# Performance work log

Hardware: AMD Instinct MI355X
Metric: run time of the kernel (lower is better)

## Reference

```python
import jax, jax.numpy as jnp
import numpy as np

B, N, C, NSAMPLE = 4, 1024, 512, 32
RADIUS, HMIN, HMAX = 0.05, -0.02, 0.04
EPS = 1e-5


def setup_inputs() -> dict:
    key = jax.random.key(0)
    ks = jax.random.split(key, 6)
    # points in a ~20cm cube so the 5cm cylinder actually captures neighbors
    seed_xyz_graspable = jax.random.uniform(ks[0], (B, N, 3), jnp.float32) * 0.2
    seed_features_graspable = jax.random.normal(ks[1], (B, C, N), jnp.float32)
    rot_raw = jax.random.normal(ks[2], (B, N, 3, 3), jnp.float32)
    vp_rot, _ = jnp.linalg.qr(rot_raw)  # proper-ish per-seed view rotations
    W1 = jax.random.normal(ks[3], (512, 3 + C), jnp.float32) / np.float32(np.sqrt(3 + C))
    g1 = jnp.ones((512,), jnp.float32)
    b1 = jnp.zeros((512,), jnp.float32)
    W2 = jax.random.normal(ks[4], (512, 512), jnp.float32) / np.float32(np.sqrt(512))
    g2 = jnp.ones((512,), jnp.float32)
    b2 = jnp.zeros((512,), jnp.float32)
    return dict(seed_xyz_graspable=seed_xyz_graspable,
                seed_features_graspable=seed_features_graspable,
                vp_rot=vp_rot, W1=W1, g1=g1, b1=b1, W2=W2, g2=g2, b2=b2)


def _cylinder_query(xyz, rot):
    # offsets d[b,m,n] = xyz[b,n] - query[b,m], rotated into the cylinder frame (d @ R)
    d = xyz[:, None, :, :] - xyz[:, :, None, :]                 # (B,M,N,3)
    r = jnp.einsum('bmnd,bmde->bmne', d, rot)                   # (B,M,N,3)
    mask = (r[..., 1] ** 2 + r[..., 2] ** 2 < RADIUS ** 2) \
         & (r[..., 0] > HMIN) & (r[..., 0] < HMAX)              # (B,M,N)
    # first NSAMPLE valid indices; pad with the first valid index (CUDA kernel semantics)
    cand = jnp.where(mask, jnp.arange(N, dtype=jnp.int32)[None, None, :], N)
    idx = jnp.sort(cand, axis=-1)[..., :NSAMPLE]                # (B,M,S)
    idx = jnp.where(idx == N, idx[..., :1], idx)
    return idx


def _bn_relu(x, g, b):
    # training-mode BatchNorm2d over (B, M, S) per output channel; x: (B,O,M,S)
    mean = jnp.mean(x, axis=(0, 2, 3), keepdims=True)
    var = jnp.var(x, axis=(0, 2, 3), keepdims=True)
    xn = (x - mean) * jax.lax.rsqrt(var + EPS)
    return jax.nn.relu(xn * g[None, :, None, None] + b[None, :, None, None])


def reference(seed_xyz_graspable, seed_features_graspable, vp_rot, W1, g1, b1, W2, g2, b2):
    xyz = seed_xyz_graspable                                    # (B,N,3)
    idx = _cylinder_query(xyz, vp_rot)                          # (B,M,S) int32
    # gather neighbor coordinates and center/rotate/normalize
    grouped_xyz = jnp.take_along_axis(xyz[:, None], idx[..., None], axis=2)   # (B,M,S,3)
    local = grouped_xyz - xyz[:, :, None, :]
    local = jnp.einsum('bmsd,bmde->bmse', local, vp_rot) / RADIUS             # normalize_xyz
    # gather neighbor features
    feats = jnp.swapaxes(seed_features_graspable, 1, 2)                       # (B,N,C)
    gfeat = jnp.take_along_axis(feats[:, None], idx[..., None], axis=2)       # (B,M,S,C)
    x = jnp.concatenate([local, gfeat], axis=-1)                              # (B,M,S,3+C)
    # SharedMLP: 1x1 conv (no bias) + BN + ReLU, twice; channels-first layout (B,O,M,S)
    h = _bn_relu(jnp.einsum('bmsc,oc->boms', x, W1), g1, b1)
    h = _bn_relu(jnp.einsum('boms,po->bpms', h, W2), g2, b2)
    # max-pool over the nsample axis -> (B,512,M)
    return jnp.max(h, axis=-1)
```

## Files before the change

kernel.cpp:

```cpp
#include <hip/hip_runtime.h>
#include <hip/hip_bf16.h>
#include <stdint.h>

#define BATCH 4
#define NPTS  1024
#define CIN   512
#define NS    32
#define P_TOT (BATCH*NPTS*NS)
#define CO    512
#define RADIUS_F 0.05f
#define HMIN_F  (-0.02f)
#define HMAX_F  (0.04f)

typedef __attribute__((ext_vector_type(8))) short short8;
typedef __attribute__((ext_vector_type(4))) float f32x4;

__device__ __forceinline__ unsigned short f2bf(float f) {
  unsigned int x = __float_as_uint(f);
  x = x + 0x7fffu + ((x >> 16) & 1u);
  return (unsigned short)(x >> 16);
}
__device__ __forceinline__ float bf2f(unsigned short u) {
  return __uint_as_float(((unsigned int)u) << 16);
}
__device__ __forceinline__ unsigned int cvtpk(float lo, float hi) {
  unsigned int r;
  asm("v_cvt_pk_bf16_f32 %0, %1, %2" : "=v"(r) : "v"(lo), "v"(hi));
  return r;
}
__device__ __forceinline__ void load_lds16(const void* g, void* l) {
  __builtin_amdgcn_global_load_lds((const __attribute__((address_space(1))) void*)g,
                                   (__attribute__((address_space(3))) void*)l, 16, 0, 0);
}

__global__ __launch_bounds__(256) void pre_kernel(
    const float* __restrict__ feats, const float* __restrict__ W1,
    const float* __restrict__ W2, const float* __restrict__ xyz,
    const float* __restrict__ rot,
    unsigned short* __restrict__ featsT, unsigned short* __restrict__ w1f,
    float* __restrict__ w1l, unsigned short* __restrict__ w2b,
    int* __restrict__ idxout, float* __restrict__ lxyz,
    float* __restrict__ L4, float* __restrict__ GMP) {
  __shared__ float tile[64][65];
  __shared__ int sidx[4][32];
  int bx = blockIdx.x;
  int t = threadIdx.x;
  if (bx < 512) {
    int nb = bx & 15, cb = (bx >> 4) & 7, b = bx >> 7;
    int tr = t >> 6, tc = t & 63;
    #pragma unroll
    for (int j = 0; j < 16; ++j) {
      int c = cb*64 + j*4 + tr;
      tile[j*4+tr][tc] = feats[((size_t)b*CIN + c)*NPTS + nb*64 + tc];
    }
    __syncthreads();
    #pragma unroll
    for (int j = 0; j < 16; ++j) {
      int n = nb*64 + j*4 + tr;
      featsT[((size_t)b*NPTS + n)*CIN + cb*64 + tc] = f2bf(tile[tc][j*4+tr]);
    }
  } else if (bx < 1536) {
    int i = (bx - 512)*256 + t;
    int o = i >> 9, k = i & 511;
    w1f[i] = f2bf(W1[o*515 + 3 + k]);
    w2b[i] = f2bf(W2[i]);
    if (i < 1536) w1l[i] = W1[(i/3)*515 + (i%3)];
  } else {
    int w = t >> 6, lane = t & 63;
    int bm = (bx - 1536)*4 + w;
    int b = bm >> 10;
    const float* ctr = xyz + (size_t)bm * 3;
    float cx = ctr[0], cy = ctr[1], cz = ctr[2];
    const float* R = rot + (size_t)bm * 9;
    float r00=R[0],r01=R[1],r02=R[2],r10=R[3],r11=R[4],r12=R[5],r20=R[6],r21=R[7],r22=R[8];
    int taken = 0;
    for (int base = 0; base < NPTS && taken < NS; base += 64) {
      int n = base + lane;
      const float* p = xyz + ((size_t)b * NPTS + n) * 3;
      float dx = p[0]-cx, dy = p[1]-cy, dz = p[2]-cz;
      float rx = dx*r00 + dy*r10 + dz*r20;
      float ry = dx*r01 + dy*r11 + dz*r21;
      float rz = dx*r02 + dy*r12 + dz*r22;
      bool ok = (ry*ry + rz*rz < RADIUS_F*RADIUS_F) && (rx > HMIN_F) && (rx < HMAX_F);
      unsigned long long bal = __ballot(ok);
      if (ok) {
        int slot = taken + __popcll(bal & ((1ull << lane) - 1ull));
        if (slot < NS) sidx[w][slot] = n;
      }
      taken += __popcll(bal);
    }
    __syncthreads();
    int filled = taken < NS ? taken : NS;
    float m[9] = {0.f,0.f,0.f,0.f,0.f,0.f,0.f,0.f,0.f};
    if (lane < NS) {
      int nsel = (lane < filled) ? sidx[w][lane] : sidx[w][0];
      size_t pp = (size_t)bm * NS + lane;
      idxout[pp] = nsel;
      const float* pn = xyz + ((size_t)b * NPTS + nsel) * 3;
      float dx = pn[0]-cx, dy = pn[1]-cy, dz = pn[2]-cz;
      const float inv = 1.0f / RADIUS_F;
      float rx = (dx*r00 + dy*r10 + dz*r20) * inv;
      float ry = (dx*r01 + dy*r11 + dz*r21) * inv;
      float rz = (dx*r02 + dy*r12 + dz*r22) * inv;
      float* lw = lxyz + pp * 3;
      lw[0] = rx; lw[1] = ry; lw[2] = rz;
      float* dst = L4 + (((size_t)b << 10) + nsel)*4;
      atomicAdd(dst+0, rx); atomicAdd(dst+1, ry);
      atomicAdd(dst+2, rz); atomicAdd(dst+3, 1.0f);
      m[0]=rx; m[1]=ry; m[2]=rz;
      m[3]=rx*rx; m[4]=rx*ry; m[5]=rx*rz; m[6]=ry*ry; m[7]=ry*rz; m[8]=rz*rz;
    }
    #pragma unroll
    for (int d = 1; d < 64; d <<= 1)
      #pragma unroll
      for (int e = 0; e < 9; ++e) m[e] += __shfl_xor(m[e], d);
    if (lane < 9) atomicAdd(&GMP[(bm & 31)*12 + lane], m[lane]);
  }
}

__global__ __launch_bounds__(256) void gemm1u_kernel(
    const unsigned short* __restrict__ A,
    const unsigned short* __restrict__ Bw,
    float* __restrict__ C,
    const float* __restrict__ L4,
    const float* __restrict__ w1l,
    float* __restrict__ sums)
{
  __shared__ unsigned short As[64*32];
  __shared__ unsigned short Bs[64*32];
  int bx = blockIdx.x;
  int ob = bx & 7;
  size_t p0 = (size_t)(bx >> 3) * 64;
  int o0 = ob * 64;
  int t = threadIdx.x;
  int w = t >> 6, lane = t & 63;
  int wr = w >> 1, wc = w & 1;
  int l15 = lane & 15, l4 = lane >> 4;
  f32x4 acc[2][2];
  f32x4 zf = {0.f, 0.f, 0.f, 0.f};
  #pragma unroll
  for (int mi = 0; mi < 2; ++mi)
    #pragma unroll
    for (int ni = 0; ni < 2; ++ni) acc[mi][ni] = zf;

  int srow = t >> 2;
  int scol = (t & 3) * 8;
  const unsigned short* abase = A + (p0 + srow)*(size_t)512 + scol;
  const unsigned short* bbase = Bw + (size_t)(o0 + srow)*512 + scol;

  for (int k0 = 0; k0 < 512; k0 += 32) {
    load_lds16(abase + k0, (char*)As + w*1024);
    load_lds16(bbase + k0, (char*)Bs + w*1024);
    __syncthreads();
    short8 af[2], bfr[2];
    #pragma unroll
    for (int mi = 0; mi < 2; ++mi)
      af[mi] = *(const short8*)(As + (wr*32 + mi*16 + l15)*32 + l4*8);
    #pragma unroll
    for (int ni = 0; ni < 2; ++ni)
      bfr[ni] = *(const short8*)(Bs + (wc*32 + ni*16 + l15)*32 + l4*8);
    #pragma unroll
    for (int mi = 0; mi < 2; ++mi)
      #pragma unroll
      for (int ni = 0; ni < 2; ++ni)
        acc[mi][ni] = __builtin_amdgcn_mfma_f32_16x16x32_bf16(af[mi], bfr[ni], acc[mi][ni], 0, 0, 0);
    __syncthreads();
  }
  #pragma unroll
  for (int mi = 0; mi < 2; ++mi)
    #pragma unroll
    for (int ni = 0; ni < 2; ++ni)
      #pragma unroll
      for (int j = 0; j < 4; ++j) {
        size_t p = p0 + wr*32 + mi*16 + l4*4 + j;
        int o = o0 + wc*32 + ni*16 + l15;
        C[p*512 + o] = acc[mi][ni][j];
      }
  #pragma unroll
  for (int ni = 0; ni < 2; ++ni) {
    int c = o0 + wc*32 + ni*16 + l15;
    float wa = w1l[c*3], wb = w1l[c*3+1], wcc = w1l[c*3+2];
    float s = 0.f, q = 0.f;
    #pragma unroll
    for (int mi = 0; mi < 2; ++mi)
      #pragma unroll
      for (int j = 0; j < 4; ++j) {
        size_t p = p0 + wr*32 + mi*16 + l4*4 + j;
        float4 L = *(const float4*)(L4 + p*4);
        float h = acc[mi][ni][j];
        float lw = L.x*wa + L.y*wb + L.z*wcc;
        s += L.w*h;
        q += L.w*h*h + 2.f*h*lw;
      }
    s += __shfl_xor(s, 16); q += __shfl_xor(q, 16);
    s += __shfl_xor(s, 32); q += __shfl_xor(q, 32);
    if (l4 == 0) {
      atomicAdd(&sums[c], s);
      atomicAdd(&sums[512 + c], q);
    }
  }
}

__global__ __launch_bounds__(256) void fold_fin_kernel(
    float* __restrict__ h1u,
    const float* __restrict__ sums,
    const float* __restrict__ GMP,
    const float* __restrict__ w1l,
    const float* __restrict__ g,
    const float* __restrict__ bia,
    float* __restrict__ w1ls) {
  __shared__ float ssl[1024];
  __shared__ float gms[9];
  int t = threadIdx.x;
  if (t < 9) {
    float s = 0.f;
    #pragma unroll
    for (int k = 0; k < 32; ++k) s += GMP[k*12 + t];
    gms[t] = s;
  }
  __syncthreads();
  #pragma unroll
  for (int cc = t; cc < 512; cc += 256) {
    float w0 = w1l[cc*3], w1 = w1l[cc*3+1], w2 = w1l[cc*3+2];
    float S = sums[cc] + w0*gms[0] + w1*gms[1] + w2*gms[2];
    float Q = sums[512+cc] + w0*w0*gms[3] + 2.f*w0*w1*gms[4] + 2.f*w0*w2*gms[5]
                           + w1*w1*gms[6] + 2.f*w1*w2*gms[7] + w2*w2*gms[8];
    const float invN = 1.f / (float)P_TOT;
    float mean = S * invN;
    float var  = Q * invN - mean*mean;
    float sc = g[cc] * rsqrtf(var + 1e-5f);
    ssl[cc] = sc;
    ssl[512+cc] = bia[cc] - mean*sc;
    if (blockIdx.x == 0) {
      w1ls[cc]        = sc * w0;
      w1ls[512 + cc]  = sc * w1;
      w1ls[1024 + cc] = sc * w2;
    }
  }
  __syncthreads();
  size_t i = ((size_t)blockIdx.x*256 + t) * 4;
  int c = (int)(i & 511);
  float4 v = *(float4*)(h1u + i);
  v.x = fmaf(v.x, ssl[c],   ssl[512+c]);
  v.y = fmaf(v.y, ssl[c+1], ssl[512+c+1]);
  v.z = fmaf(v.z, ssl[c+2], ssl[512+c+2]);
  v.w = fmaf(v.w, ssl[c+3], ssl[512+c+3]);
  *(float4*)(h1u + i) = v;
}

__global__ __launch_bounds__(512) void gemm2_kernel(
    const float* __restrict__ h1u,
    const int* __restrict__ idx,
    const float* __restrict__ lxyz,
    const float* __restrict__ w1ls,
    const unsigned short* __restrict__ Bw,
    float* __restrict__ sums,
    float* __restrict__ pmax,
    float* __restrict__ pmin)
{
  __shared__ unsigned short As[128*32];
  __shared__ unsigned short Bs[256*32];
  __shared__ float wl[1536];
  int bx = blockIdx.x;
  int ob = bx & 1;
  size_t p0 = (size_t)(bx >> 1) * 128;
  int o0 = ob * 256;
  int t = threadIdx.x;
  int w = t >> 6, lane = t & 63;
  int wr = w >> 2;
  int wc = w & 3;
  int l15 = lane & 15, l4 = lane >> 4;
  f32x4 acc[4][4];
  f32x4 zf = {0.f, 0.f, 0.f, 0.f};
  #pragma unroll
  for (int mi = 0; mi < 4; ++mi)
    #pragma unroll
    for (int ni = 0; ni < 4; ++ni) acc[mi][ni] = zf;

  int sl = (lane & 3) ^ ((lane >> 3) & 3);
  int scole = (lane & 3) * 8;
  int cA = (l4 ^ ((l15 >> 1) & 3)) * 8;

  wl[t] = w1ls[t]; wl[512 + t] = w1ls[512 + t]; wl[1024 + t] = w1ls[1024 + t];

  int arow = 16*w + (lane >> 2);
  int awoff = arow*64 + sl*16;
  const float* hptr;
  float lxr, lyr, lzr;
  {
    size_t p = p0 + arow;
    int b = (int)(p >> 15);
    int n = idx[p];
    hptr = h1u + (((size_t)b << 10) + n)*512 + scole;
    const float* lwp = lxyz + p*3;
    lxr = lwp[0]; lyr = lwp[1]; lzr = lwp[2];
  }
  const unsigned short* bptr[2];
  #pragma unroll
  for (int cc = 0; cc < 2; ++cc) {
    int brow = 16*(2*w + cc) + (lane >> 2);
    bptr[cc] = Bw + (size_t)(o0 + brow)*CIN + sl*8;
  }

  float4 hv0 = *(const float4*)(hptr);
  float4 hv1 = *(const float4*)(hptr + 4);
  __syncthreads();

  for (int k0 = 0; k0 < CIN; k0 += 32) {
    #pragma unroll
    for (int cc = 0; cc < 2; ++cc)
      load_lds16(bptr[cc] + k0, (char*)Bs + (2*w + cc)*1024);
    int ch0 = k0 + scole;
    float4 xa = *(const float4*)(wl + ch0);
    float4 xb = *(const float4*)(wl + ch0 + 4);
    float4 ya = *(const float4*)(wl + 512 + ch0);
    float4 yb = *(const float4*)(wl + 512 + ch0 + 4);
    float4 za = *(const float4*)(wl + 1024 + ch0);
    float4 zb = *(const float4*)(wl + 1024 + ch0 + 4);
    float w0[8] = {xa.x,xa.y,xa.z,xa.w,xb.x,xb.y,xb.z,xb.w};
    float w1[8] = {ya.x,ya.y,ya.z,ya.w,yb.x,yb.y,yb.z,yb.w};
    float w2[8] = {za.x,za.y,za.z,za.w,zb.x,zb.y,zb.z,zb.w};
    {
      float fv[8] = {hv0.x, hv0.y, hv0.z, hv0.w, hv1.x, hv1.y, hv1.z, hv1.w};
      float gv[8];
      #pragma unroll
      for (int e = 0; e < 8; ++e)
        gv[e] = fmaxf(fv[e] + lxr*w0[e] + lyr*w1[e] + lzr*w2[e], 0.f);
      unsigned int rv[4];
      #pragma unroll
      for (int j = 0; j < 4; ++j) rv[j] = cvtpk(gv[2*j], gv[2*j+1]);
      *(uint4*)((char*)As + awoff) = make_uint4(rv[0], rv[1], rv[2], rv[3]);
    }
    if (k0 + 32 < CIN) {
      hv0 = *(const float4*)(hptr + k0 + 32);
      hv1 = *(const float4*)(hptr + k0 + 36);
    }
    __syncthreads();
    short8 af[4], bfr[4];
    #pragma unroll
    for (int mi = 0; mi < 4; ++mi)
      af[mi] = *(const short8*)(As + (wr*64 + mi*16 + l15)*32 + cA);
    #pragma unroll
    for (int ni = 0; ni < 4; ++ni)
      bfr[ni] = *(const short8*)(Bs + (wc*64 + ni*16 + l15)*32 + cA);
    #pragma unroll
    for (int mi = 0; mi < 4; ++mi)
      #pragma unroll
      for (int ni = 0; ni < 4; ++ni)
        acc[mi][ni] = __builtin_amdgcn_mfma_f32_16x16x32_bf16(af[mi], bfr[ni], acc[mi][ni], 0, 0, 0);
    __syncthreads();
  }

  #pragma unroll
  for (int ni = 0; ni < 4; ++ni) {
    float s = 0.f, q = 0.f;
    #pragma unroll
    for (int mi = 0; mi < 4; ++mi)
      #pragma unroll
      for (int j = 0; j < 4; ++j) { float v = acc[mi][ni][j]; s += v; q += v*v; }
    s += __shfl_xor(s, 16); q += __shfl_xor(q, 16);
    s += __shfl_xor(s, 32); q += __shfl_xor(q, 32);
    if (l4 == 0) {
      int c = o0 + wc*64 + ni*16 + l15;
      atomicAdd(&sums[c], s);
      atomicAdd(&sums[512 + c], q);
    }
  }
  #pragma unroll
  for (int ni = 0; ni < 4; ++ni) {
    #pragma unroll
    for (int h = 0; h < 2; ++h) {
      float mx = -3.4e38f, mn = 3.4e38f;
      #pragma unroll
      for (int mi = 2*h; mi < 2*h + 2; ++mi)
        #pragma unroll
        for (int j = 0; j < 4; ++j) {
          float v = acc[mi][ni][j];
          mx = fmaxf(mx, v); mn = fminf(mn, v);
        }
      mx = fmaxf(mx, __shfl_xor(mx, 16)); mn = fminf(mn, __shfl_xor(mn, 16));
      mx = fmaxf(mx, __shfl_xor(mx, 32)); mn = fminf(mn, __shfl_xor(mn, 32));
      if (l4 == 0) {
        size_t bm = (p0 >> 5) + 2*wr + h;
        int o = o0 + wc*64 + ni*16 + l15;
        pmax[bm*512 + o] = mx;
        pmin[bm*512 + o] = mn;
      }
    }
  }
}

__global__ void final_transpose(const float* __restrict__ pmax,
                                const float* __restrict__ pmin,
                                const float* __restrict__ sums,
                                const float* __restrict__ g,
                                const float* __restrict__ bia,
                                float* __restrict__ out) {
  __shared__ float tile[64][65];
  __shared__ float scl[64], shl[64];
  int b = blockIdx.z, ob = blockIdx.y, mb = blockIdx.x;
  int t = threadIdx.x, tr = t >> 6, tc = t & 63;
  if (t < 64) {
    int c = ob*64 + t;
    const float invN = 1.f / (float)P_TOT;
    float mean = sums[c] * invN;
    float var  = sums[512+c] * invN - mean*mean;
    float sc = g[c] * rsqrtf(var + 1e-5f);
    scl[t] = sc;
    shl[t] = bia[c] - mean*sc;
  }
  __syncthreads();
  #pragma unroll
  for (int j = 0; j < 16; ++j) {
    int m = mb*64 + j*4 + tr;
    float sc = scl[tc], sh = shl[tc];
    size_t pi = (((size_t)b << 10) + m)*512 + ob*64 + tc;
    float v = (sc >= 0.f) ? pmax[pi] : pmin[pi];
    tile[j*4+tr][tc] = fmaxf(fmaf(v, sc, sh), 0.f);
  }
  __syncthreads();
  #pragma unroll
  for (int j = 0; j < 16; ++j) {
    int o = ob*64 + j*4 + tr;
    out[((size_t)b*512 + o)*1024 + mb*64 + tc] = tile[tc][j*4+tr];
  }
}

extern "C" void kernel_launch(void* const* d_in, const int* in_sizes, int n_in,
                              void* d_out, int out_size, void* d_ws, size_t ws_size,
                              hipStream_t stream) {
  const float* xyz   = (const float*)d_in[0];
  const float* feats = (const float*)d_in[1];
  const float* rot   = (const float*)d_in[2];
  const float* W1    = (const float*)d_in[3];
  const float* g1    = (const float*)d_in[4];
  const float* b1    = (const float*)d_in[5];
  const float* W2    = (const float*)d_in[6];
  const float* g2    = (const float*)d_in[7];
  const float* b2    = (const float*)d_in[8];
  float* out = (float*)d_out;
  char* wsb = (char*)d_ws;

  const size_t OFF_IDX    = 0;
  const size_t OFF_LXYZ   = OFF_IDX    + (size_t)P_TOT*4;
  const size_t OFF_FEATST = OFF_LXYZ   + (size_t)P_TOT*3*4;
  const size_t OFF_W1F    = OFF_FEATST + (size_t)BATCH*NPTS*CIN*2;
  const size_t OFF_W1L    = OFF_W1F    + (size_t)CO*512*2;
  const size_t OFF_W1LS   = OFF_W1L    + 8192;
  const size_t OFF_W2B    = OFF_W1LS   + 8192;
  const size_t OFF_STATS  = OFF_W2B    + (size_t)CO*CIN*2;
  const size_t OFF_L4     = OFF_STATS  + 16384;
  const size_t OFF_GMP    = OFF_L4     + 65536;
  const size_t OFF_H1U    = OFF_GMP    + 4096;
  const size_t OFF_PMAX   = OFF_H1U    + (size_t)BATCH*NPTS*CO*4;
  const size_t OFF_PMIN   = OFF_PMAX   + (size_t)BATCH*NPTS*CO*4;
  const size_t WS_NEED    = OFF_PMIN   + (size_t)BATCH*NPTS*CO*4;

  if (ws_size < WS_NEED) return;

  int* idx             = (int*)(wsb + OFF_IDX);
  float* lxyz          = (float*)(wsb + OFF_LXYZ);
  unsigned short* fT   = (unsigned short*)(wsb + OFF_FEATST);
  unsigned short* w1f  = (unsigned short*)(wsb + OFF_W1F);
  float* w1l           = (float*)(wsb + OFF_W1L);
  float* w1ls          = (float*)(wsb + OFF_W1LS);
  unsigned short* w2b  = (unsigned short*)(wsb + OFF_W2B);
  float* stats         = (float*)(wsb + OFF_STATS);
  float* sums1 = stats;
  float* sums2 = stats + 2048;
  float* L4            = (float*)(wsb + OFF_L4);
  float* GMP           = (float*)(wsb + OFF_GMP);
  float* h1u           = (float*)(wsb + OFF_H1U);
  float* pmax          = (float*)(wsb + OFF_PMAX);
  float* pmin          = (float*)(wsb + OFF_PMIN);

  hipMemsetAsync(stats, 0, 16384 + 65536 + 4096, stream);

  pre_kernel<<<2560, 256, 0, stream>>>(feats, W1, W2, xyz, rot,
                                       fT, w1f, w1l, w2b, idx, lxyz, L4, GMP);

  gemm1u_kernel<<<512, 256, 0, stream>>>(fT, w1f, h1u, L4, w1l, sums1);

  fold_fin_kernel<<<(BATCH*NPTS*CO/4)/256, 256, 0, stream>>>(h1u, sums1, GMP,
                                                             w1l, g1, b1, w1ls);

  gemm2_kernel<<<(P_TOT/128)*2, 512, 0, stream>>>(h1u, idx, lxyz, w1ls, w2b,
                                                  sums2, pmax, pmin);

  final_transpose<<<dim3(NPTS/64, CO/64, BATCH), 256, 0, stream>>>(pmax, pmin,
                                                                   sums2, g2, b2, out);
}
```

Baseline: 194.1 us.

## Double-buffer B tile and prefetch A inputs two steps ahead in gemm2

Splits the LDS B tile into two buffers so the next K-slice's weights load asynchronously while MFMAs run on the current slice. The A-tile transform for the next slice is computed in registers during the current iteration, and the global h1 loads are issued two steps ahead. The goal is to hide global-to-LDS latency behind matrix math. In exchange the B tile uses twice the LDS, register pressure rises, and each iteration still has two barriers because As is single-buffered.

```diff
diff --git a/kernel.cpp b/kernel.cpp
--- a/kernel.cpp
+++ b/kernel.cpp
@@ -259,7 +259,7 @@
     float* __restrict__ pmin)
 {
   __shared__ unsigned short As[128*32];
-  __shared__ unsigned short Bs[256*32];
+  __shared__ unsigned short Bs[2][256*32];
   __shared__ float wl[1536];
   int bx = blockIdx.x;
   int ob = bx & 1;
@@ -302,15 +302,7 @@
     bptr[cc] = Bw + (size_t)(o0 + brow)*CIN + sl*8;
   }
 
-  float4 hv0 = *(const float4*)(hptr);
-  float4 hv1 = *(const float4*)(hptr + 4);
-  __syncthreads();
-
-  for (int k0 = 0; k0 < CIN; k0 += 32) {
-    #pragma unroll
-    for (int cc = 0; cc < 2; ++cc)
-      load_lds16(bptr[cc] + k0, (char*)Bs + (2*w + cc)*1024);
-    int ch0 = k0 + scole;
+  auto xform = [&](const float4& a, const float4& b, int ch0, unsigned int* rv) {
     float4 xa = *(const float4*)(wl + ch0);
     float4 xb = *(const float4*)(wl + ch0 + 4);
     float4 ya = *(const float4*)(wl + 512 + ch0);
@@ -320,35 +312,62 @@
     float w0[8] = {xa.x,xa.y,xa.z,xa.w,xb.x,xb.y,xb.z,xb.w};
     float w1[8] = {ya.x,ya.y,ya.z,ya.w,yb.x,yb.y,yb.z,yb.w};
     float w2[8] = {za.x,za.y,za.z,za.w,zb.x,zb.y,zb.z,zb.w};
-    {
-      float fv[8] = {hv0.x, hv0.y, hv0.z, hv0.w, hv1.x, hv1.y, hv1.z, hv1.w};
-      float gv[8];
-      #pragma unroll
-      for (int e = 0; e < 8; ++e)
-        gv[e] = fmaxf(fv[e] + lxr*w0[e] + lyr*w1[e] + lzr*w2[e], 0.f);
-      unsigned int rv[4];
-      #pragma unroll
-      for (int j = 0; j < 4; ++j) rv[j] = cvtpk(gv[2*j], gv[2*j+1]);
-      *(uint4*)((char*)As + awoff) = make_uint4(rv[0], rv[1], rv[2], rv[3]);
-    }
-    if (k0 + 32 < CIN) {
-      hv0 = *(const float4*)(hptr + k0 + 32);
-      hv1 = *(const float4*)(hptr + k0 + 36);
-    }
-    __syncthreads();
+    float fv[8] = {a.x, a.y, a.z, a.w, b.x, b.y, b.z, b.w};
+    float gv[8];
+    #pragma unroll
+    for (int e = 0; e < 8; ++e)
+      gv[e] = fmaxf(fv[e] + lxr*w0[e] + lyr*w1[e] + lzr*w2[e], 0.f);
+    #pragma unroll
+    for (int j = 0; j < 4; ++j) rv[j] = cvtpk(gv[2*j], gv[2*j+1]);
+  };
+
+  #pragma unroll
+  for (int cc = 0; cc < 2; ++cc)
+    load_lds16(bptr[cc], (char*)&Bs[0][0] + (2*w + cc)*1024);
+  float4 hv0 = *(const float4*)(hptr);
+  float4 hv1 = *(const float4*)(hptr + 4);
+  __syncthreads();
+  {
+    unsigned int rv[4];
+    xform(hv0, hv1, scole, rv);
+    *(uint4*)((char*)As + awoff) = make_uint4(rv[0], rv[1], rv[2], rv[3]);
+  }
+  hv0 = *(const float4*)(hptr + 32);
+  hv1 = *(const float4*)(hptr + 36);
+  __syncthreads();
+
+  int cur = 0;
+  for (int kt = 0; kt < 16; ++kt) {
+    int k0 = kt*32;
+    if (kt < 15) {
+      #pragma unroll
+      for (int cc = 0; cc < 2; ++cc)
+        load_lds16(bptr[cc] + k0 + 32, (char*)&Bs[cur^1][0] + (2*w + cc)*1024);
+    }
+    float4 hp0, hp1;
+    if (kt < 14) {
+      hp0 = *(const float4*)(hptr + k0 + 64);
+      hp1 = *(const float4*)(hptr + k0 + 68);
+    }
     short8 af[4], bfr[4];
     #pragma unroll
     for (int mi = 0; mi < 4; ++mi)
       af[mi] = *(const short8*)(As + (wr*64 + mi*16 + l15)*32 + cA);
     #pragma unroll
     for (int ni = 0; ni < 4; ++ni)
-      bfr[ni] = *(const short8*)(Bs + (wc*64 + ni*16 + l15)*32 + cA);
+      bfr[ni] = *(const short8*)(&Bs[cur][(wc*64 + ni*16 + l15)*32 + cA]);
     #pragma unroll
     for (int mi = 0; mi < 4; ++mi)
       #pragma unroll
       for (int ni = 0; ni < 4; ++ni)
         acc[mi][ni] = __builtin_amdgcn_mfma_f32_16x16x32_bf16(af[mi], bfr[ni], acc[mi][ni], 0, 0, 0);
+    unsigned int rv[4];
+    if (kt < 15) xform(hv0, hv1, k0 + 32 + scole, rv);
     __syncthreads();
+    if (kt < 15) *(uint4*)((char*)As + awoff) = make_uint4(rv[0], rv[1], rv[2], rv[3]);
+    __syncthreads();
+    if (kt < 14) { hv0 = hp0; hv1 = hp1; }
+    cur ^= 1;
   }
 
   #pragma unroll
```

Result: slower. 225.7 us (+16.3%).
